# Kernel optimization log

Hardware: AMD Instinct MI355X
Metric: run time of the kernel (lower is better)

The kernel has to match this reference:

```python
import jax, jax.numpy as jnp
import numpy as np

N, E = 50000, 800000
H, C = 4, 32          # heads, channels -> concat dim 128
ED = 8                # edge_dim
NREL = 16             # n_relations
LAYERS = 3
MLP_HID = 100
NEG_SLOPE = 0.2


def setup_inputs():
    key = jax.random.key(0)
    ks = jax.random.split(key, 16)
    s = 0.1
    return {
        "x": jax.random.normal(ks[0], (N, 1), jnp.float32),
        "edge_index": jax.random.randint(ks[1], (2, E), 0, N),
        "edge_type": jax.random.randint(ks[2], (E,), 0, NREL),
        "edge_emb": jax.random.normal(ks[3], (NREL, ED), jnp.float32) * s,
        "W_l0": jax.random.normal(ks[4], (C, H * C), jnp.float32) * s,
        "W_l1": jax.random.normal(ks[5], (H * C, H * C), jnp.float32) * s,
        "W_l2": jax.random.normal(ks[6], (H * C, H * C), jnp.float32) * s,
        "att_src": jax.random.normal(ks[7], (LAYERS, H, C), jnp.float32) * s,
        "att_dst": jax.random.normal(ks[8], (LAYERS, H, C), jnp.float32) * s,
        "att_edge": jax.random.normal(ks[9], (LAYERS, H, C), jnp.float32) * s,
        "W_edge": jax.random.normal(ks[10], (LAYERS, ED, H * C), jnp.float32) * s,
        "bias": jax.random.normal(ks[11], (LAYERS, H * C), jnp.float32) * s,
        "mlp_W1": jax.random.normal(ks[12], (H * C, MLP_HID), jnp.float32) * s,
        "mlp_b1": jnp.zeros((MLP_HID,), jnp.float32),
        "mlp_W2": jax.random.normal(ks[13], (MLP_HID, 1), jnp.float32) * s,
        "mlp_b2": jnp.zeros((1,), jnp.float32),
    }


def _gat_layer(x, src, dst, edge_attr, W, a_src, a_dst, a_edge, We, b):
    # PyG GATConv: shared lin for src/dst, additive attention + edge attr term
    n = x.shape[0]
    h = (x @ W).reshape(n, H, C)                      # [N,H,C]
    e = (edge_attr @ We).reshape(-1, H, C)            # [E',H,C]
    s_src = (h * a_src).sum(-1)                       # [N,H]
    s_dst = (h * a_dst).sum(-1)                       # [N,H]
    s_edge = (e * a_edge).sum(-1)                     # [E',H]
    alpha = jax.nn.leaky_relu(s_src[src] + s_dst[dst] + s_edge, NEG_SLOPE)
    # softmax over incoming edges of each destination node
    amax = jax.ops.segment_max(alpha, dst, num_segments=n)
    ealpha = jnp.exp(alpha - amax[dst])
    denom = jax.ops.segment_sum(ealpha, dst, num_segments=n)
    alpha = ealpha / (denom[dst] + 1e-16)             # [E',H]
    msg = h[src] * alpha[:, :, None]                  # [E',H,C]
    out = jax.ops.segment_sum(msg, dst, num_segments=n)
    return out.reshape(n, H * C) + b


def _forward(x, edge_index, edge_type, edge_emb, W_l0, W_l1, W_l2,
             att_src, att_dst, att_edge, W_edge, bias,
             mlp_W1, mlp_b1, mlp_W2, mlp_b2):
    n = x.shape[0]
    x = jnp.broadcast_to(x, (n, C))                   # x.expand(-1, channels)
    src, dst = edge_index[0], edge_index[1]
    loop = jnp.arange(n)
    src_f = jnp.concatenate([src, loop])              # add_self_loops
    dst_f = jnp.concatenate([dst, loop])
    Ws = [W_l0, W_l1, W_l2]
    for i in range(LAYERS):
        edge_attr = edge_emb[edge_type]               # [E,ED]
        fill = jnp.broadcast_to(edge_attr.mean(0), (n, ED))  # fill_value='mean'
        edge_attr_f = jnp.concatenate([edge_attr, fill], axis=0)
        xl = x
        x = _gat_layer(x, src_f, dst_f, edge_attr_f, Ws[i],
                       att_src[i], att_dst[i], att_edge[i], W_edge[i], bias[i])
        if i > 0:
            x = x + xl                                # residual (i>0 only)
        x = jax.nn.relu(x)                            # nonlin; norm='none'
    h = jax.nn.relu(x @ mlp_W1 + mlp_b1)
    return jax.nn.sigmoid(h @ mlp_W2 + mlp_b2)        # [N,1]


def reference(x, edge_index, edge_type, edge_emb, W_l0, W_l1, W_l2,
              att_src, att_dst, att_edge, W_edge, bias,
              mlp_W1, mlp_b1, mlp_W2, mlp_b2):
    return _forward(x, edge_index, edge_type, edge_emb, W_l0, W_l1, W_l2,
                    att_src, att_dst, att_edge, W_edge, bias,
                    mlp_W1, mlp_b1, mlp_W2, mlp_b2)
```

## Files before the change

kernel.cpp:

```cpp
#include <hip/hip_runtime.h>
#include <hip/hip_bf16.h>
#include <hip/hip_fp16.h>

#define HCONC 128
#define NHEAD 4
#define CCH   32
#define EDIM  8
#define NREL  16
#define BCAP  5120
#define TILE  2048

typedef float floatx2 __attribute__((ext_vector_type(2)));
typedef short bf16x8 __attribute__((ext_vector_type(8)));
typedef float f32x4 __attribute__((ext_vector_type(4)));

__device__ inline unsigned short pack_fp8x2(float a, float b) {
    return (unsigned short)(__builtin_amdgcn_cvt_pk_fp8_f32(a, b, 0, false) & 0xFFFF);
}
__device__ inline unsigned pack_bf2(float lo, float hi) {
    __hip_bfloat162 v;
    v.x = __float2bfloat16(lo);
    v.y = __float2bfloat16(hi);
    return *(unsigned*)&v;
}

__global__ __launch_bounds__(256) void binA_kernel(
    const int* __restrict__ ei, const int* __restrict__ etype, int E, int nbuk, int nA,
    int* __restrict__ gcursor, int* __restrict__ cnt, unsigned* __restrict__ ebuf,
    const float* __restrict__ W_l1, const float* __restrict__ W_l2,
    const float* __restrict__ mW1,
    unsigned* __restrict__ Wl1q, unsigned* __restrict__ Wl2q, unsigned* __restrict__ W1q,
    const float* __restrict__ W_l0, const float* __restrict__ emb,
    const float* __restrict__ att_src, const float* __restrict__ att_dst,
    const float* __restrict__ att_edge, const float* __restrict__ W_edge,
    float* __restrict__ W0s, float* __restrict__ SA0, float* __restrict__ SD0,
    float* __restrict__ stab) {
    __shared__ int hist[256], lbase[256], gbase[256], tmp[256];
    __shared__ int lcnt16[NREL];
    __shared__ unsigned srt[TILE];
    __shared__ unsigned char sbuk[TILE];
    __shared__ float W0s_s[HCONC];
    int t = threadIdx.x;

    if ((int)blockIdx.x >= nA) {
        int pb = (int)blockIdx.x - nA;
        if (pb == 92) {
            if (t < HCONC) {
                float s = 0.f;
                for (int k = 0; k < CCH; k++) s += W_l0[k * HCONC + t];
                W0s[t] = s; W0s_s[t] = s;
            }
            __syncthreads();
            if (t < NHEAD) {
                float sa = 0.f, sd = 0.f;
                for (int c = 0; c < CCH; c++) {
                    sa += W0s_s[t * CCH + c] * att_src[t * CCH + c];
                    sd += W0s_s[t * CCH + c] * att_dst[t * CCH + c];
                }
                SA0[t] = sa; SD0[t] = sd;
            }
            if (t < 192) {
                int l = t >> 6, rem = t & 63, typ = rem >> 2, hh = rem & 3;
                const float* attr = emb + typ * EDIM;
                const float* We = W_edge + l * EDIM * HCONC;
                const float* ae = att_edge + l * HCONC + hh * CCH;
                float s = 0.f;
                for (int c = 0; c < CCH; c++) {
                    float ev = 0.f;
                    for (int dd = 0; dd < EDIM; dd++)
                        ev += attr[dd] * We[dd * HCONC + hh * CCH + c];
                    s += ev * ae[c];
                }
                stab[l * 68 + typ * 4 + hh] = s;
            }
            return;
        }
        int i = pb * 256 + t;
        if (i < 16384) {
            const float* W = (i < 8192) ? W_l1 : W_l2;
            unsigned* dst = (i < 8192) ? Wl1q : Wl2q;
            int r = i & 8191;
            int j2 = r & 3, lane = (r >> 2) & 63, kb = (r >> 8) & 3, tt = r >> 10;
            int k0 = kb * 32 + ((lane >> 4) & 3) * 8 + 2 * j2;
            int c = 16 * tt + (lane & 15);
            dst[r] = pack_bf2(W[k0 * 128 + c], W[(k0 + 1) * 128 + c]);
        } else if (i < 16384 + 7168) {
            int r = i - 16384;
            int j2 = r & 3, lane = (r >> 2) & 63, kb = (r >> 8) & 3, tt = r >> 10;
            int k0 = kb * 32 + ((lane >> 4) & 3) * 8 + 2 * j2;
            int c = 16 * tt + (lane & 15);
            float lo = (c < 100) ? mW1[k0 * 100 + c] : 0.f;
            float hi = (c < 100) ? mW1[(k0 + 1) * 100 + c] : 0.f;
            W1q[r] = pack_bf2(lo, hi);
        }
        return;
    }

    hist[t] = 0;
    if (t < NREL) lcnt16[t] = 0;
    __syncthreads();

    int base = blockIdx.x * TILE;
    int count = min(TILE, E - base);

    unsigned rec[8]; int slot[8]; int buk[8];
#pragma unroll
    for (int i = 0; i < 8; i++) {
        int idx = t + i * 256;
        if (idx < count) {
            int g = base + idx;
            int s = ei[g], d = ei[E + g], ty = etype[g];
            rec[i] = (unsigned)s | ((unsigned)ty << 16) | ((unsigned)(d & 255) << 20);
            buk[i] = d >> 8;
            slot[i] = atomicAdd(&hist[buk[i]], 1);
            atomicAdd(&lcnt16[ty], 1);
        } else buk[i] = -1;
    }
    __syncthreads();

    int v = hist[t];
    tmp[t] = v; __syncthreads();
    for (int off = 1; off < 256; off <<= 1) {
        int add = (t >= off) ? tmp[t - off] : 0; __syncthreads();
        tmp[t] += add; __syncthreads();
    }
    lbase[t] = tmp[t] - v;
    if (t < nbuk && v > 0) gbase[t] = atomicAdd(&gcursor[t], v);
    __syncthreads();

#pragma unroll
    for (int i = 0; i < 8; i++)
        if (buk[i] >= 0) {
            int pos = lbase[buk[i]] + slot[i];
            srt[pos] = rec[i];
            sbuk[pos] = (unsigned char)buk[i];
        }
    if (t < NREL) atomicAdd(&cnt[t], lcnt16[t]);
    __syncthreads();

    for (int idx = t; idx < count; idx += 256) {
        unsigned r = srt[idx];
        int bk = sbuk[idx];
        int rel = gbase[bk] + idx - lbase[bk];
        if (rel < BCAP) ebuf[bk * BCAP + rel] = r;
    }
}

__global__ __launch_bounds__(256) void binB_kernel(
    const unsigned* __restrict__ ebuf, const int* __restrict__ gcursor,
    int n, int nbuk,
    int* __restrict__ row_ptr, unsigned* __restrict__ col,
    const int* __restrict__ cnt, float* __restrict__ stab, int E,
    const float* __restrict__ x,
    const float* __restrict__ SA0, const float* __restrict__ SD0,
    float* __restrict__ val0) {
    __shared__ int hist[256], lcur[256], tmp[256];
    __shared__ unsigned colsl[BCAP];
    __shared__ __align__(16) float stab0[68];
    int b = blockIdx.x, t = threadIdx.x;

    if (t < 64) stab0[t] = stab[t];
    float invE = 1.f / (float)E;
    if (t < 4) {
        float s = 0.f;
        for (int r = 0; r < NREL; r++) s += (float)cnt[r] * stab[r * 4 + t];
        stab0[64 + t] = s * invE;
    }

    int c = (t < nbuk) ? gcursor[t] : 0;
    tmp[t] = c; __syncthreads();
    for (int off = 1; off < 256; off <<= 1) {
        int add = (t >= off) ? tmp[t - off] : 0; __syncthreads();
        tmp[t] += add; __syncthreads();
    }
    int gstart = (b == 0) ? 0 : tmp[b - 1];
    if (b == 0 && t == nbuk - 1) row_ptr[n] = tmp[t];
    if (b == 0 && t < 12) {
        int l = t >> 2, hh = t & 3;
        float s = 0.f;
        for (int r = 0; r < NREL; r++) s += (float)cnt[r] * stab[l * 68 + r * 4 + hh];
        stab[l * 68 + 64 + hh] = s * invE;
    }
    __syncthreads();

    int bbase = b * BCAP;
    int cntb = min(gcursor[b], BCAP);
    hist[t] = 0;
    __syncthreads();
    for (int i = t; i < cntb; i += 256) {
        unsigned r = ebuf[bbase + i];
        atomicAdd(&hist[r >> 20], 1);
    }
    __syncthreads();
    int v = hist[t];
    tmp[t] = v; __syncthreads();
    for (int off = 1; off < 256; off <<= 1) {
        int add = (t >= off) ? tmp[t - off] : 0; __syncthreads();
        tmp[t] += add; __syncthreads();
    }
    lcur[t] = tmp[t] - v;
    int gdst = (b << 8) + t;
    if (gdst < n) row_ptr[gdst] = gstart + tmp[t] - v;
    __syncthreads();
    for (int i = t; i < cntb; i += 256) {
        unsigned r = ebuf[bbase + i];
        int pos = atomicAdd(&lcur[r >> 20], 1);
        colsl[pos] = r & 0xFFFFFu;
    }
    __syncthreads();
    for (int i = t; i < cntb; i += 256)
        col[gstart + i] = colsl[i];

    int lo = tmp[t] - v, hi = tmp[t];
    if (gdst < n) {
        float xd = x[gdst];
        float4 sa4 = *(const float4*)SA0;
        float4 sdc = *(const float4*)SD0;
        float sd0 = xd * sdc.x, sd1 = xd * sdc.y, sd2 = xd * sdc.z, sd3 = xd * sdc.w;
        float s0 = fmaf(xd, sa4.x, sd0) + stab0[64];
        float s1 = fmaf(xd, sa4.y, sd1) + stab0[65];
        float s2 = fmaf(xd, sa4.z, sd2) + stab0[66];
        float s3 = fmaf(xd, sa4.w, sd3) + stab0[67];
        s0 = s0 > 0.f ? s0 : 0.2f * s0;
        s1 = s1 > 0.f ? s1 : 0.2f * s1;
        s2 = s2 > 0.f ? s2 : 0.2f * s2;
        s3 = s3 > 0.f ? s3 : 0.2f * s3;
        float w0 = __expf(s0), w1 = __expf(s1), w2 = __expf(s2), w3 = __expf(s3);
        float den0 = w0, den1 = w1, den2 = w2, den3 = w3;
        float sx0 = w0 * xd, sx1 = w1 * xd, sx2 = w2 * xd, sx3 = w3 * xd;
        for (int j = lo; j < hi; j++) {
            unsigned p = colsl[j];
            float xv = x[p & 0xFFFFu];
            int typ = (int)(p >> 16);
            float4 st = *(const float4*)&stab0[typ * 4];
            float e0 = fmaf(xv, sa4.x, sd0) + st.x;
            float e1 = fmaf(xv, sa4.y, sd1) + st.y;
            float e2 = fmaf(xv, sa4.z, sd2) + st.z;
            float e3 = fmaf(xv, sa4.w, sd3) + st.w;
            e0 = e0 > 0.f ? e0 : 0.2f * e0;
            e1 = e1 > 0.f ? e1 : 0.2f * e1;
            e2 = e2 > 0.f ? e2 : 0.2f * e2;
            e3 = e3 > 0.f ? e3 : 0.2f * e3;
            float g0 = __expf(e0), g1 = __expf(e1), g2 = __expf(e2), g3 = __expf(e3);
            den0 += g0; den1 += g1; den2 += g2; den3 += g3;
            sx0 = fmaf(g0, xv, sx0); sx1 = fmaf(g1, xv, sx1);
            sx2 = fmaf(g2, xv, sx2); sx3 = fmaf(g3, xv, sx3);
        }
        float4 vo;
        vo.x = sx0 / (den0 + 1e-16f);
        vo.y = sx1 / (den1 + 1e-16f);
        vo.z = sx2 / (den2 + 1e-16f);
        vo.w = sx3 / (den3 + 1e-16f);
        ((float4*)val0)[gdst] = vo;
    }
}

__global__ __launch_bounds__(256, 2) void transform0_kernel(
    const float* __restrict__ val0, const float* __restrict__ W0s,
    const float* __restrict__ bias0, const unsigned* __restrict__ Wq,
    const float* __restrict__ a_src, const float* __restrict__ a_dst,
    unsigned short* __restrict__ h8, float* __restrict__ s_src,
    float* __restrict__ s_dst, int n) {
    __shared__ unsigned short hs[64 * 128];
    int tid = threadIdx.x;
    int lane = tid & 63;
    int wv = tid >> 6;
    int q = lane >> 4, nl = lane & 15;
    int row_blk = blockIdx.x * 64;
    int wrow = wv * 16;

    int arow = row_blk + wrow + nl;
    if (arow >= n) arow = n - 1;
    float4 v4 = ((const float4*)val0)[arow];

    f32x4 acc[8];
#pragma unroll
    for (int t = 0; t < 8; t++) acc[t] = (f32x4){0.f, 0.f, 0.f, 0.f};

    const uint4* Wp4 = (const uint4*)Wq;
#pragma unroll
    for (int kb = 0; kb < 4; kb++) {
        int c4 = 8 * kb + 2 * q;
        float4 wa = ((const float4*)W0s)[c4];
        float4 wb = ((const float4*)W0s)[c4 + 1];
        float4 ba = ((const float4*)bias0)[c4];
        float4 bb = ((const float4*)bias0)[c4 + 1];
        float vr = kb == 0 ? v4.x : kb == 1 ? v4.y : kb == 2 ? v4.z : v4.w;
        float x0 = fmaxf(fmaf(vr, wa.x, ba.x), 0.f);
        float x1 = fmaxf(fmaf(vr, wa.y, ba.y), 0.f);
        float x2 = fmaxf(fmaf(vr, wa.z, ba.z), 0.f);
        float x3 = fmaxf(fmaf(vr, wa.w, ba.w), 0.f);
        float x4 = fmaxf(fmaf(vr, wb.x, bb.x), 0.f);
        float x5 = fmaxf(fmaf(vr, wb.y, bb.y), 0.f);
        float x6 = fmaxf(fmaf(vr, wb.z, bb.z), 0.f);
        float x7 = fmaxf(fmaf(vr, wb.w, bb.w), 0.f);
        uint4 ua;
        ua.x = pack_bf2(x0, x1);
        ua.y = pack_bf2(x2, x3);
        ua.z = pack_bf2(x4, x5);
        ua.w = pack_bf2(x6, x7);
        bf16x8 af = __builtin_bit_cast(bf16x8, ua);
#pragma unroll
        for (int t = 0; t < 8; t++) {
            uint4 ub = Wp4[(t * 4 + kb) * 64 + lane];
            bf16x8 bf = __builtin_bit_cast(bf16x8, ub);
            acc[t] = __builtin_amdgcn_mfma_f32_16x16x32_bf16(af, bf, acc[t], 0, 0, 0);
        }
    }

    float av[8], dv[8];
#pragma unroll
    for (int t = 0; t < 8; t++) {
        av[t] = a_src[16 * t + nl];
        dv[t] = a_dst[16 * t + nl];
    }
#pragma unroll
    for (int reg = 0; reg < 4; reg++) {
        float t0 = acc[0][reg] * av[0] + acc[1][reg] * av[1];
        float t1 = acc[2][reg] * av[2] + acc[3][reg] * av[3];
        float t2 = acc[4][reg] * av[4] + acc[5][reg] * av[5];
        float t3 = acc[6][reg] * av[6] + acc[7][reg] * av[7];
        float d0 = acc[0][reg] * dv[0] + acc[1][reg] * dv[1];
        float d1 = acc[2][reg] * dv[2] + acc[3][reg] * dv[3];
        float d2 = acc[4][reg] * dv[4] + acc[5][reg] * dv[5];
        float d3 = acc[6][reg] * dv[6] + acc[7][reg] * dv[7];
#pragma unroll
        for (int off = 1; off <= 8; off <<= 1) {
            t0 += __shfl_xor(t0, off); t1 += __shfl_xor(t1, off);
            t2 += __shfl_xor(t2, off); t3 += __shfl_xor(t3, off);
            d0 += __shfl_xor(d0, off); d1 += __shfl_xor(d1, off);
            d2 += __shfl_xor(d2, off); d3 += __shfl_xor(d3, off);
        }
        int row = row_blk + wrow + q * 4 + reg;
        if (row < n && nl < 4) {
            float ts = nl == 0 ? t0 : nl == 1 ? t1 : nl == 2 ? t2 : t3;
            float td = nl == 0 ? d0 : nl == 1 ? d1 : nl == 2 ? d2 : d3;
            s_src[row * 4 + nl] = ts;
            s_dst[row * 4 + nl] = td;
        }
    }

#pragma unroll
    for (int t = 0; t < 8; t++) {
#pragma unroll
        for (int reg = 0; reg < 4; reg++) {
            __hip_bfloat16 b = __float2bfloat16(acc[t][reg]);
            hs[(wrow + q * 4 + reg) * 128 + 16 * t + nl] = *(unsigned short*)&b;
        }
    }
    __syncthreads();
    const unsigned* hsu = (const unsigned*)hs;
#pragma unroll
    for (int i = 0; i < 16; i++) {
        int pidx = tid + i * 256;
        int rl = pidx >> 6, cp = pidx & 63;
        int row = row_blk + rl;
        if (row < n) {
            unsigned u = hsu[rl * 64 + cp];
            float f0 = __uint_as_float(u << 16);
            float f1 = __uint_as_float(u & 0xFFFF0000u);
            h8[(size_t)row * 64 + cp] = pack_fp8x2(f0, f1);
        }
    }
}

__global__ __launch_bounds__(256, 2) void transform_kernel(
    const unsigned short* __restrict__ Xbf, const unsigned* __restrict__ Wq,
    const float* __restrict__ a_src, const float* __restrict__ a_dst,
    unsigned short* __restrict__ h8, float* __restrict__ s_src,
    float* __restrict__ s_dst, int n) {
    __shared__ unsigned short hs[64 * 128];
    int tid = threadIdx.x;
    int lane = tid & 63;
    int wv = tid >> 6;
    int q = lane >> 4, nl = lane & 15;
    int row_blk = blockIdx.x * 64;
    int wrow = wv * 16;

    int arow = row_blk + wrow + nl;
    if (arow >= n) arow = n - 1;
    const uint4* Xr = (const uint4*)(Xbf + (size_t)arow * HCONC);

    f32x4 acc[8];
#pragma unroll
    for (int t = 0; t < 8; t++) acc[t] = (f32x4){0.f, 0.f, 0.f, 0.f};

    const uint4* Wp4 = (const uint4*)Wq;
#pragma unroll
    for (int kb = 0; kb < 4; kb++) {
        uint4 ua = Xr[kb * 4 + q];
        bf16x8 af = __builtin_bit_cast(bf16x8, ua);
#pragma unroll
        for (int t = 0; t < 8; t++) {
            uint4 ub = Wp4[(t * 4 + kb) * 64 + lane];
            bf16x8 bf = __builtin_bit_cast(bf16x8, ub);
            acc[t] = __builtin_amdgcn_mfma_f32_16x16x32_bf16(af, bf, acc[t], 0, 0, 0);
        }
    }

    float av[8], dv[8];
#pragma unroll
    for (int t = 0; t < 8; t++) {
        av[t] = a_src[16 * t + nl];
        dv[t] = a_dst[16 * t + nl];
    }
#pragma unroll
    for (int reg = 0; reg < 4; reg++) {
        float t0 = acc[0][reg] * av[0] + acc[1][reg] * av[1];
        float t1 = acc[2][reg] * av[2] + acc[3][reg] * av[3];
        float t2 = acc[4][reg] * av[4] + acc[5][reg] * av[5];
        float t3 = acc[6][reg] * av[6] + acc[7][reg] * av[7];
        float d0 = acc[0][reg] * dv[0] + acc[1][reg] * dv[1];
        float d1 = acc[2][reg] * dv[2] + acc[3][reg] * dv[3];
        float d2 = acc[4][reg] * dv[4] + acc[5][reg] * dv[5];
        float d3 = acc[6][reg] * dv[6] + acc[7][reg] * dv[7];
#pragma unroll
        for (int off = 1; off <= 8; off <<= 1) {
            t0 += __shfl_xor(t0, off); t1 += __shfl_xor(t1, off);
            t2 += __shfl_xor(t2, off); t3 += __shfl_xor(t3, off);
            d0 += __shfl_xor(d0, off); d1 += __shfl_xor(d1, off);
            d2 += __shfl_xor(d2, off); d3 += __shfl_xor(d3, off);
        }
        int row = row_blk + wrow + q * 4 + reg;
        if (row < n && nl < 4) {
            float ts = nl == 0 ? t0 : nl == 1 ? t1 : nl == 2 ? t2 : t3;
            float td = nl == 0 ? d0 : nl == 1 ? d1 : nl == 2 ? d2 : d3;
            s_src[row * 4 + nl] = ts;
            s_dst[row * 4 + nl] = td;
        }
    }

#pragma unroll
    for (int t = 0; t < 8; t++) {
#pragma unroll
        for (int reg = 0; reg < 4; reg++) {
            __hip_bfloat16 b = __float2bfloat16(acc[t][reg]);
            hs[(wrow + q * 4 + reg) * 128 + 16 * t + nl] = *(unsigned short*)&b;
        }
    }
    __syncthreads();
    const unsigned* hsu = (const unsigned*)hs;
#pragma unroll
    for (int i = 0; i < 16; i++) {
        int pidx = tid + i * 256;
        int rl = pidx >> 6, cp = pidx & 63;
        int row = row_blk + rl;
        if (row < n) {
            unsigned u = hsu[rl * 64 + cp];
            float f0 = __uint_as_float(u << 16);
            float f1 = __uint_as_float(u & 0xFFFF0000u);
            h8[(size_t)row * 64 + cp] = pack_fp8x2(f0, f1);
        }
    }
}

template <bool VAL_RES, bool OUT_BF16, bool RES_BF16>
__global__ __launch_bounds__(256) void agg_kernel(
    const unsigned char* __restrict__ h8,
    const float* __restrict__ s_src, const float* __restrict__ s_dst,
    const int* __restrict__ row_ptr, const unsigned* __restrict__ col,
    const float* __restrict__ tab, const float* __restrict__ bias,
    const void* __restrict__ x_prev,
    const float* __restrict__ val0, const float* __restrict__ W0s,
    const float* __restrict__ bias0,
    void* __restrict__ x_out, int n) {
    __shared__ __align__(16) float stab_s[68];
    if (threadIdx.x < 68) stab_s[threadIdx.x] = tab[threadIdx.x];
    __syncthreads();

    int tid = threadIdx.x;
    int lane = tid & 63;
    int grp = lane >> 4;
    int l16 = lane & 15;
    int head = l16 >> 2;
    int d = blockIdx.x * 16 + (tid >> 6) * 4 + grp;
    if (d >= n) return;

    int start = row_ptr[d], end = row_ptr[d + 1];
    float sdh = s_dst[d * 4 + head];

    float s = s_src[d * 4 + head] + sdh + stab_s[64 + head];
    s = s > 0.f ? s : 0.2f * s;
    float w = __expf(s);
    uint2 u = ((const uint2*)(h8 + (size_t)d * 128))[l16];
    floatx2 f01 = __builtin_amdgcn_cvt_pk_f32_fp8((int)u.x, false);
    floatx2 f23 = __builtin_amdgcn_cvt_pk_f32_fp8((int)u.x, true);
    floatx2 f45 = __builtin_amdgcn_cvt_pk_f32_fp8((int)u.y, false);
    floatx2 f67 = __builtin_amdgcn_cvt_pk_f32_fp8((int)u.y, true);
    float den = w;
    float a0 = w * f01.x, a1 = w * f01.y;
    float a2 = w * f23.x, a3 = w * f23.y;
    float a4 = w * f45.x, a5 = w * f45.y;
    float a6 = w * f67.x, a7 = w * f67.y;

#pragma unroll 4
    for (int e = start; e < end; e++) {
        unsigned pp = col[e];
        int esrc = (int)(pp & 0xFFFFu);
        int typ = (int)(pp >> 16);
        float ss = s_src[esrc * 4 + head];
        float sc = ss + sdh + stab_s[typ * 4 + head];
        sc = sc > 0.f ? sc : 0.2f * sc;
        float we = __expf(sc);
        uint2 ue = ((const uint2*)(h8 + (size_t)esrc * 128))[l16];
        floatx2 g01 = __builtin_amdgcn_cvt_pk_f32_fp8((int)ue.x, false);
        floatx2 g23 = __builtin_amdgcn_cvt_pk_f32_fp8((int)ue.x, true);
        floatx2 g45 = __builtin_amdgcn_cvt_pk_f32_fp8((int)ue.y, false);
        floatx2 g67 = __builtin_amdgcn_cvt_pk_f32_fp8((int)ue.y, true);
        den += we;
        a0 = fmaf(we, g01.x, a0);  a1 = fmaf(we, g01.y, a1);
        a2 = fmaf(we, g23.x, a2);  a3 = fmaf(we, g23.y, a3);
        a4 = fmaf(we, g45.x, a4);  a5 = fmaf(we, g45.y, a5);
        a6 = fmaf(we, g67.x, a6);  a7 = fmaf(we, g67.y, a7);
    }

    float inv = 1.f / (den + 1e-16f);
    float4 b0 = ((const float4*)bias)[2 * l16];
    float4 b1v = ((const float4*)bias)[2 * l16 + 1];
    float4 o0v, o1v;
    o0v.x = a0 * inv + b0.x;  o0v.y = a1 * inv + b0.y;
    o0v.z = a2 * inv + b0.z;  o0v.w = a3 * inv + b0.w;
    o1v.x = a4 * inv + b1v.x; o1v.y = a5 * inv + b1v.y;
    o1v.z = a6 * inv + b1v.z; o1v.w = a7 * inv + b1v.w;
    if (VAL_RES) {
        float vv = val0[d * 4 + head];
        float4 wa = ((const float4*)W0s)[2 * l16];
        float4 wb = ((const float4*)W0s)[2 * l16 + 1];
        float4 ba = ((const float4*)bias0)[2 * l16];
        float4 bb = ((const float4*)bias0)[2 * l16 + 1];
        o0v.x += fmaxf(fmaf(vv, wa.x, ba.x), 0.f);
        o0v.y += fmaxf(fmaf(vv, wa.y, ba.y), 0.f);
        o0v.z += fmaxf(fmaf(vv, wa.z, ba.z), 0.f);
        o0v.w += fmaxf(fmaf(vv, wa.w, ba.w), 0.f);
        o1v.x += fmaxf(fmaf(vv, wb.x, bb.x), 0.f);
        o1v.y += fmaxf(fmaf(vv, wb.y, bb.y), 0.f);
        o1v.z += fmaxf(fmaf(vv, wb.z, bb.z), 0.f);
        o1v.w += fmaxf(fmaf(vv, wb.w, bb.w), 0.f);
    } else if (RES_BF16) {
        uint4 pk = ((const uint4*)x_prev)[(size_t)d * 16 + l16];
        o0v.x += __uint_as_float(pk.x << 16);
        o0v.y += __uint_as_float(pk.x & 0xFFFF0000u);
        o0v.z += __uint_as_float(pk.y << 16);
        o0v.w += __uint_as_float(pk.y & 0xFFFF0000u);
        o1v.x += __uint_as_float(pk.z << 16);
        o1v.y += __uint_as_float(pk.z & 0xFFFF0000u);
        o1v.z += __uint_as_float(pk.w << 16);
        o1v.w += __uint_as_float(pk.w & 0xFFFF0000u);
    }
    o0v.x = fmaxf(o0v.x, 0.f); o0v.y = fmaxf(o0v.y, 0.f);
    o0v.z = fmaxf(o0v.z, 0.f); o0v.w = fmaxf(o0v.w, 0.f);
    o1v.x = fmaxf(o1v.x, 0.f); o1v.y = fmaxf(o1v.y, 0.f);
    o1v.z = fmaxf(o1v.z, 0.f); o1v.w = fmaxf(o1v.w, 0.f);
    if (OUT_BF16) {
        uint4 pk;
        pk.x = pack_bf2(o0v.x, o0v.y);
        pk.y = pack_bf2(o0v.z, o0v.w);
        pk.z = pack_bf2(o1v.x, o1v.y);
        pk.w = pack_bf2(o1v.z, o1v.w);
        ((uint4*)x_out)[(size_t)d * 16 + l16] = pk;
    } else {
        ((float4*)x_out)[(size_t)d * 32 + 2 * l16]     = o0v;
        ((float4*)x_out)[(size_t)d * 32 + 2 * l16 + 1] = o1v;
    }
}

__global__ __launch_bounds__(256, 2) void mlp_kernel(
    const unsigned short* __restrict__ Xbf, const unsigned* __restrict__ W1q,
    const float* __restrict__ b1, const float* __restrict__ W2,
    const float* __restrict__ b2, float* __restrict__ out, int n) {
    int tid = threadIdx.x;
    int lane = tid & 63;
    int wv = tid >> 6;
    int q = lane >> 4, nl = lane & 15;
    int row_blk = blockIdx.x * 64;
    int wrow = wv * 16;

    int arow = row_blk + wrow + nl;
    if (arow >= n) arow = n - 1;
    const uint4* Xr = (const uint4*)(Xbf + (size_t)arow * HCONC);

    f32x4 acc[7];
#pragma unroll
    for (int t = 0; t < 7; t++) acc[t] = (f32x4){0.f, 0.f, 0.f, 0.f};

    const uint4* Wp4 = (const uint4*)W1q;
#pragma unroll
    for (int kb = 0; kb < 4; kb++) {
        uint4 ua = Xr[kb * 4 + q];
        bf16x8 af = __builtin_bit_cast(bf16x8, ua);
#pragma unroll
        for (int t = 0; t < 7; t++) {
            uint4 ub = Wp4[(t * 4 + kb) * 64 + lane];
            bf16x8 bf = __builtin_bit_cast(bf16x8, ub);
            acc[t] = __builtin_amdgcn_mfma_f32_16x16x32_bf16(af, bf, acc[t], 0, 0, 0);
        }
    }

    float b1c[7], w2c[7];
#pragma unroll
    for (int t = 0; t < 7; t++) {
        int c = 16 * t + nl;
        bool vld = c < 100;
        b1c[t] = vld ? b1[c] : 0.f;
        w2c[t] = vld ? W2[c] : 0.f;
    }
    float b2v = b2[0];

#pragma unroll
    for (int reg = 0; reg < 4; reg++) {
        float sum = 0.f;
#pragma unroll
        for (int t = 0; t < 7; t++) {
            float hv = fmaxf(acc[t][reg] + b1c[t], 0.f);
            sum = fmaf(hv, w2c[t], sum);
        }
#pragma unroll
        for (int off = 1; off <= 8; off <<= 1)
            sum += __shfl_xor(sum, off);
        int row = row_blk + wrow + q * 4 + reg;
        if (nl == 0 && row < n)
            out[row] = 1.f / (1.f + __expf(-(sum + b2v)));
    }
}

extern "C" void kernel_launch(void* const* d_in, const int* in_sizes, int n_in,
                              void* d_out, int out_size, void* d_ws, size_t ws_size,
                              hipStream_t stream) {
    const float* x       = (const float*)d_in[0];
    const int*   ei      = (const int*)d_in[1];
    const int*   etype   = (const int*)d_in[2];
    const float* emb     = (const float*)d_in[3];
    const float* W_l0    = (const float*)d_in[4];
    const float* W_l1    = (const float*)d_in[5];
    const float* W_l2    = (const float*)d_in[6];
    const float* att_src = (const float*)d_in[7];
    const float* att_dst = (const float*)d_in[8];
    const float* att_edge= (const float*)d_in[9];
    const float* W_edge  = (const float*)d_in[10];
    const float* bias    = (const float*)d_in[11];
    const float* mW1     = (const float*)d_in[12];
    const float* mb1     = (const float*)d_in[13];
    const float* mW2     = (const float*)d_in[14];
    const float* mb2     = (const float*)d_in[15];

    int n = in_sizes[0];
    int E = in_sizes[2];
    int nbuk = (n + 255) >> 8;
    int nA = (E + TILE - 1) / TILE;

    float* p   = (float*)d_ws;
    float* xa  = p; p += (size_t)n * HCONC;
    float* xb  = p; p += (size_t)n * HCONC;
    float* ssrc = p; p += (size_t)n * NHEAD;
    float* sdst = p; p += (size_t)n * NHEAD;
    float* val0 = p; p += (size_t)n * NHEAD;
    float* hbf  = p; p += (size_t)n * 32;
    unsigned* Wl1q = (unsigned*)p; p += 8192;
    unsigned* Wl2q = (unsigned*)p; p += 8192;
    unsigned* W1q  = (unsigned*)p; p += 7168;
    int* row_ptr     = (int*)p;
    int* gcursor     = row_ptr + n + 1;
    int* cnt         = gcursor + 256;
    float* W0s    = (float*)(cnt + 16);
    float* SA0    = W0s + HCONC;
    float* SD0    = SA0 + NHEAD;
    float* meanat = SD0 + NHEAD;
    float* stab   = meanat + EDIM;
    char* raw = (char*)(stab + 256);
    unsigned* ebuf = (unsigned*)(((uintptr_t)raw + 15) & ~(uintptr_t)15);
    unsigned* col = ebuf + (size_t)nbuk * BCAP;

    hipMemsetAsync(gcursor, 0, (256 + 16) * sizeof(int), stream);
    binA_kernel<<<nA + 93, 256, 0, stream>>>(ei, etype, E, nbuk, nA, gcursor, cnt,
                                             ebuf, W_l1, W_l2, mW1, Wl1q, Wl2q, W1q,
                                             W_l0, emb, att_src, att_dst, att_edge,
                                             W_edge, W0s, SA0, SD0, stab);
    binB_kernel<<<nbuk, 256, 0, stream>>>(ebuf, gcursor, n, nbuk, row_ptr, col,
                                          cnt, stab, E, x, SA0, SD0, val0);

    transform0_kernel<<<(n + 63) / 64, 256, 0, stream>>>(val0, W0s, bias + 0, Wl1q,
                                                         att_src + 128, att_dst + 128,
                                                         (unsigned short*)hbf, ssrc, sdst, n);
    agg_kernel<true, true, false><<<(n + 15) / 16, 256, 0, stream>>>(
        (const unsigned char*)hbf, ssrc, sdst, row_ptr, col,
        stab + 68, bias + 128, nullptr, val0, W0s, bias + 0, xb, n);
    transform_kernel<<<(n + 63) / 64, 256, 0, stream>>>((const unsigned short*)xb, Wl2q,
                                                        att_src + 256, att_dst + 256,
                                                        (unsigned short*)hbf, ssrc, sdst, n);
    agg_kernel<false, true, true><<<(n + 15) / 16, 256, 0, stream>>>(
        (const unsigned char*)hbf, ssrc, sdst, row_ptr, col,
        stab + 136, bias + 256, xb, nullptr, nullptr, nullptr, xa, n);
    mlp_kernel<<<(n + 63) / 64, 256, 0, stream>>>((const unsigned short*)xa, W1q,
                                                  mb1, mW2, mb2, (float*)d_out, n);
}
```

Before: 220.4 us.

## Fuse layer-2 transform into agg epilogue and MLP into final aggregation

The layer-1 aggregation kernel now stages its 16 output rows in shared memory and immediately runs the layer-2 MFMA transform, attention-score reduction and fp8 packing. This removes the separate transform kernel and its re-read of the bf16 activations. The final aggregation likewise computes the MLP head and sigmoid in-block, dropping the xa buffer and the mlp kernel. Separate double buffers for h8 and the scores avoid read/write hazards between blocks. The trade-offs are extra syncthreads and more shared memory per block in the latency-bound gather kernels, plus 16-row MFMA tiles that reload weights more often.

```diff
diff --git a/kernel.cpp b/kernel.cpp
--- a/kernel.cpp
+++ b/kernel.cpp
@@ -364,125 +364,42 @@
     }
 }
 
-__global__ __launch_bounds__(256, 2) void transform_kernel(
-    const unsigned short* __restrict__ Xbf, const unsigned* __restrict__ Wq,
-    const float* __restrict__ a_src, const float* __restrict__ a_dst,
-    unsigned short* __restrict__ h8, float* __restrict__ s_src,
-    float* __restrict__ s_dst, int n) {
-    __shared__ unsigned short hs[64 * 128];
+__global__ __launch_bounds__(256) void agg_t_kernel(
+    const unsigned char* __restrict__ h8, const float* __restrict__ s_src,
+    const float* __restrict__ s_dst, const int* __restrict__ row_ptr,
+    const unsigned* __restrict__ col, const float* __restrict__ tab,
+    const float* __restrict__ bias, const float* __restrict__ val0,
+    const float* __restrict__ W0s, const float* __restrict__ bias0,
+    unsigned short* __restrict__ xb_out,
+    const unsigned* __restrict__ Wq,
+    const float* __restrict__ a_src2, const float* __restrict__ a_dst2,
+    unsigned short* __restrict__ h8o, float* __restrict__ s_srco,
+    float* __restrict__ s_dsto, int n) {
+    __shared__ __align__(16) float stab_s[68];
+    __shared__ __align__(16) unsigned short xrow[16 * 144];
+    __shared__ __align__(4) unsigned short hs[16 * 130];
+    if (threadIdx.x < 68) stab_s[threadIdx.x] = tab[threadIdx.x];
+    __syncthreads();
+
     int tid = threadIdx.x;
     int lane = tid & 63;
     int wv = tid >> 6;
-    int q = lane >> 4, nl = lane & 15;
-    int row_blk = blockIdx.x * 64;
-    int wrow = wv * 16;
-
-    int arow = row_blk + wrow + nl;
-    if (arow >= n) arow = n - 1;
-    const uint4* Xr = (const uint4*)(Xbf + (size_t)arow * HCONC);
-
-    f32x4 acc[8];
-#pragma unroll
-    for (int t = 0; t < 8; t++) acc[t] = (f32x4){0.f, 0.f, 0.f, 0.f};
-
-    const uint4* Wp4 = (const uint4*)Wq;
-#pragma unroll
-    for (int kb = 0; kb < 4; kb++) {
-        uint4 ua = Xr[kb * 4 + q];
-        bf16x8 af = __builtin_bit_cast(bf16x8, ua);
-#pragma unroll
-        for (int t = 0; t < 8; t++) {
-            uint4 ub = Wp4[(t * 4 + kb) * 64 + lane];
-            bf16x8 bf = __builtin_bit_cast(bf16x8, ub);
-            acc[t] = __builtin_amdgcn_mfma_f32_16x16x32_bf16(af, bf, acc[t], 0, 0, 0);
-        }
-    }
-
-    float av[8], dv[8];
-#pragma unroll
-    for (int t = 0; t < 8; t++) {
-        av[t] = a_src[16 * t + nl];
-        dv[t] = a_dst[16 * t + nl];
-    }
-#pragma unroll
-    for (int reg = 0; reg < 4; reg++) {
-        float t0 = acc[0][reg] * av[0] + acc[1][reg] * av[1];
-        float t1 = acc[2][reg] * av[2] + acc[3][reg] * av[3];
-        float t2 = acc[4][reg] * av[4] + acc[5][reg] * av[5];
-        float t3 = acc[6][reg] * av[6] + acc[7][reg] * av[7];
-        float d0 = acc[0][reg] * dv[0] + acc[1][reg] * dv[1];
-        float d1 = acc[2][reg] * dv[2] + acc[3][reg] * dv[3];
-        float d2 = acc[4][reg] * dv[4] + acc[5][reg] * dv[5];
-        float d3 = acc[6][reg] * dv[6] + acc[7][reg] * dv[7];
-#pragma unroll
-        for (int off = 1; off <= 8; off <<= 1) {
-            t0 += __shfl_xor(t0, off); t1 += __shfl_xor(t1, off);
-            t2 += __shfl_xor(t2, off); t3 += __shfl_xor(t3, off);
-            d0 += __shfl_xor(d0, off); d1 += __shfl_xor(d1, off);
-            d2 += __shfl_xor(d2, off); d3 += __shfl_xor(d3, off);
-        }
-        int row = row_blk + wrow + q * 4 + reg;
-        if (row < n && nl < 4) {
-            float ts = nl == 0 ? t0 : nl == 1 ? t1 : nl == 2 ? t2 : t3;
-            float td = nl == 0 ? d0 : nl == 1 ? d1 : nl == 2 ? d2 : d3;
-            s_src[row * 4 + nl] = ts;
-            s_dst[row * 4 + nl] = td;
-        }
-    }
-
-#pragma unroll
-    for (int t = 0; t < 8; t++) {
-#pragma unroll
-        for (int reg = 0; reg < 4; reg++) {
-            __hip_bfloat16 b = __float2bfloat16(acc[t][reg]);
-            hs[(wrow + q * 4 + reg) * 128 + 16 * t + nl] = *(unsigned short*)&b;
-        }
-    }
-    __syncthreads();
-    const unsigned* hsu = (const unsigned*)hs;
-#pragma unroll
-    for (int i = 0; i < 16; i++) {
-        int pidx = tid + i * 256;
-        int rl = pidx >> 6, cp = pidx & 63;
-        int row = row_blk + rl;
-        if (row < n) {
-            unsigned u = hsu[rl * 64 + cp];
-            float f0 = __uint_as_float(u << 16);
-            float f1 = __uint_as_float(u & 0xFFFF0000u);
-            h8[(size_t)row * 64 + cp] = pack_fp8x2(f0, f1);
-        }
-    }
-}
-
-template <bool VAL_RES, bool OUT_BF16, bool RES_BF16>
-__global__ __launch_bounds__(256) void agg_kernel(
-    const unsigned char* __restrict__ h8,
-    const float* __restrict__ s_src, const float* __restrict__ s_dst,
-    const int* __restrict__ row_ptr, const unsigned* __restrict__ col,
-    const float* __restrict__ tab, const float* __restrict__ bias,
-    const void* __restrict__ x_prev,
-    const float* __restrict__ val0, const float* __restrict__ W0s,
-    const float* __restrict__ bias0,
-    void* __restrict__ x_out, int n) {
-    __shared__ __align__(16) float stab_s[68];
-    if (threadIdx.x < 68) stab_s[threadIdx.x] = tab[threadIdx.x];
-    __syncthreads();
-
-    int tid = threadIdx.x;
-    int lane = tid & 63;
     int grp = lane >> 4;
     int l16 = lane & 15;
     int head = l16 >> 2;
-    int d = blockIdx.x * 16 + (tid >> 6) * 4 + grp;
-    if (d >= n) return;
-
-    int start = row_ptr[d], end = row_ptr[d + 1];
-    float sdh = s_dst[d * 4 + head];
-
-    float s = s_src[d * 4 + head] + sdh + stab_s[64 + head];
+    int dl = wv * 4 + grp;
+    int d = blockIdx.x * 16 + dl;
+    bool alive = d < n;
+    int dc = alive ? d : n - 1;
+
+    int start = row_ptr[dc];
+    int end = alive ? row_ptr[dc + 1] : start;
+    float sdh = s_dst[dc * 4 + head];
+
+    float s = s_src[dc * 4 + head] + sdh + stab_s[64 + head];
     s = s > 0.f ? s : 0.2f * s;
     float w = __expf(s);
-    uint2 u = ((const uint2*)(h8 + (size_t)d * 128))[l16];
+    uint2 u = ((const uint2*)(h8 + (size_t)dc * 128))[l16];
     floatx2 f01 = __builtin_amdgcn_cvt_pk_f32_fp8((int)u.x, false);
     floatx2 f23 = __builtin_amdgcn_cvt_pk_f32_fp8((int)u.x, true);
     floatx2 f45 = __builtin_amdgcn_cvt_pk_f32_fp8((int)u.y, false);
@@ -492,14 +409,12 @@
     float a2 = w * f23.x, a3 = w * f23.y;
     float a4 = w * f45.x, a5 = w * f45.y;
     float a6 = w * f67.x, a7 = w * f67.y;
-
 #pragma unroll 4
     for (int e = start; e < end; e++) {
         unsigned pp = col[e];
         int esrc = (int)(pp & 0xFFFFu);
         int typ = (int)(pp >> 16);
-        float ss = s_src[esrc * 4 + head];
-        float sc = ss + sdh + stab_s[typ * 4 + head];
+        float sc = s_src[esrc * 4 + head] + sdh + stab_s[typ * 4 + head];
         sc = sc > 0.f ? sc : 0.2f * sc;
         float we = __expf(sc);
         uint2 ue = ((const uint2*)(h8 + (size_t)esrc * 128))[l16];
@@ -522,8 +437,8 @@
     o0v.z = a2 * inv + b0.z;  o0v.w = a3 * inv + b0.w;
     o1v.x = a4 * inv + b1v.x; o1v.y = a5 * inv + b1v.y;
     o1v.z = a6 * inv + b1v.z; o1v.w = a7 * inv + b1v.w;
-    if (VAL_RES) {
-        float vv = val0[d * 4 + head];
+    {
+        float vv = val0[dc * 4 + head];
         float4 wa = ((const float4*)W0s)[2 * l16];
         float4 wb = ((const float4*)W0s)[2 * l16 + 1];
         float4 ba = ((const float4*)bias0)[2 * l16];
@@ -536,90 +451,204 @@
         o1v.y += fmaxf(fmaf(vv, wb.y, bb.y), 0.f);
         o1v.z += fmaxf(fmaf(vv, wb.z, bb.z), 0.f);
         o1v.w += fmaxf(fmaf(vv, wb.w, bb.w), 0.f);
-    } else if (RES_BF16) {
-        uint4 pk = ((const uint4*)x_prev)[(size_t)d * 16 + l16];
-        o0v.x += __uint_as_float(pk.x << 16);
-        o0v.y += __uint_as_float(pk.x & 0xFFFF0000u);
-        o0v.z += __uint_as_float(pk.y << 16);
-        o0v.w += __uint_as_float(pk.y & 0xFFFF0000u);
-        o1v.x += __uint_as_float(pk.z << 16);
-        o1v.y += __uint_as_float(pk.z & 0xFFFF0000u);
-        o1v.z += __uint_as_float(pk.w << 16);
-        o1v.w += __uint_as_float(pk.w & 0xFFFF0000u);
     }
     o0v.x = fmaxf(o0v.x, 0.f); o0v.y = fmaxf(o0v.y, 0.f);
     o0v.z = fmaxf(o0v.z, 0.f); o0v.w = fmaxf(o0v.w, 0.f);
     o1v.x = fmaxf(o1v.x, 0.f); o1v.y = fmaxf(o1v.y, 0.f);
     o1v.z = fmaxf(o1v.z, 0.f); o1v.w = fmaxf(o1v.w, 0.f);
-    if (OUT_BF16) {
-        uint4 pk;
-        pk.x = pack_bf2(o0v.x, o0v.y);
-        pk.y = pack_bf2(o0v.z, o0v.w);
-        pk.z = pack_bf2(o1v.x, o1v.y);
-        pk.w = pack_bf2(o1v.z, o1v.w);
-        ((uint4*)x_out)[(size_t)d * 16 + l16] = pk;
-    } else {
-        ((float4*)x_out)[(size_t)d * 32 + 2 * l16]     = o0v;
-        ((float4*)x_out)[(size_t)d * 32 + 2 * l16 + 1] = o1v;
+    uint4 pk;
+    pk.x = pack_bf2(o0v.x, o0v.y);
+    pk.y = pack_bf2(o0v.z, o0v.w);
+    pk.z = pack_bf2(o1v.x, o1v.y);
+    pk.w = pack_bf2(o1v.z, o1v.w);
+    if (alive) ((uint4*)xb_out)[(size_t)d * 16 + l16] = pk;
+    *(uint4*)&xrow[dl * 144 + l16 * 8] = pk;
+    __syncthreads();
+
+    int lo = 2 * wv, hi = lo + 1;
+    f32x4 aL = (f32x4){0.f, 0.f, 0.f, 0.f};
+    f32x4 aH = (f32x4){0.f, 0.f, 0.f, 0.f};
+    const uint4* Wp4 = (const uint4*)Wq;
+#pragma unroll
+    for (int kb = 0; kb < 4; kb++) {
+        bf16x8 af = __builtin_bit_cast(bf16x8,
+            *(const uint4*)&xrow[l16 * 144 + kb * 32 + grp * 8]);
+        bf16x8 bL = __builtin_bit_cast(bf16x8, Wp4[(lo * 4 + kb) * 64 + lane]);
+        bf16x8 bH = __builtin_bit_cast(bf16x8, Wp4[(hi * 4 + kb) * 64 + lane]);
+        aL = __builtin_amdgcn_mfma_f32_16x16x32_bf16(af, bL, aL, 0, 0, 0);
+        aH = __builtin_amdgcn_mfma_f32_16x16x32_bf16(af, bH, aH, 0, 0, 0);
+    }
+    float avl = a_src2[32 * wv + l16], avh = a_src2[32 * wv + 16 + l16];
+    float dvl = a_dst2[32 * wv + l16], dvh = a_dst2[32 * wv + 16 + l16];
+#pragma unroll
+    for (int reg = 0; reg < 4; reg++) {
+        float ps = aL[reg] * avl + aH[reg] * avh;
+        float pd = aL[reg] * dvl + aH[reg] * dvh;
+#pragma unroll
+        for (int off = 1; off <= 8; off <<= 1) {
+            ps += __shfl_xor(ps, off);
+            pd += __shfl_xor(pd, off);
+        }
+        int rg = blockIdx.x * 16 + grp * 4 + reg;
+        if (l16 == 0 && rg < n) {
+            s_srco[rg * 4 + wv] = ps;
+            s_dsto[rg * 4 + wv] = pd;
+        }
+        __hip_bfloat16 bLh = __float2bfloat16(aL[reg]);
+        __hip_bfloat16 bHh = __float2bfloat16(aH[reg]);
+        hs[(grp * 4 + reg) * 130 + 16 * lo + l16] = *(unsigned short*)&bLh;
+        hs[(grp * 4 + reg) * 130 + 16 * hi + l16] = *(unsigned short*)&bHh;
+    }
+    __syncthreads();
+#pragma unroll
+    for (int i = 0; i < 4; i++) {
+        int pidx = tid + i * 256;
+        int rl = pidx >> 6, cp = pidx & 63;
+        int rg = blockIdx.x * 16 + rl;
+        if (rg < n) {
+            unsigned uu = *(const unsigned*)&hs[rl * 130 + cp * 2];
+            float f0 = __uint_as_float(uu << 16);
+            float f1 = __uint_as_float(uu & 0xFFFF0000u);
+            h8o[(size_t)rg * 64 + cp] = pack_fp8x2(f0, f1);
+        }
     }
 }
 
-__global__ __launch_bounds__(256, 2) void mlp_kernel(
-    const unsigned short* __restrict__ Xbf, const unsigned* __restrict__ W1q,
-    const float* __restrict__ b1, const float* __restrict__ W2,
-    const float* __restrict__ b2, float* __restrict__ out, int n) {
+__global__ __launch_bounds__(256) void agg_m_kernel(
+    const unsigned char* __restrict__ h8, const float* __restrict__ s_src,
+    const float* __restrict__ s_dst, const int* __restrict__ row_ptr,
+    const unsigned* __restrict__ col, const float* __restrict__ tab,
+    const float* __restrict__ bias, const unsigned short* __restrict__ x_prev,
+    const unsigned* __restrict__ W1q, const float* __restrict__ b1,
+    const float* __restrict__ W2, const float* __restrict__ b2,
+    float* __restrict__ out, int n) {
+    __shared__ __align__(16) float stab_s[68];
+    __shared__ __align__(16) unsigned short xrow[16 * 144];
+    __shared__ float partial[16][4];
+    if (threadIdx.x < 68) stab_s[threadIdx.x] = tab[threadIdx.x];
+    __syncthreads();
+
     int tid = threadIdx.x;
     int lane = tid & 63;
     int wv = tid >> 6;
-    int q = lane >> 4, nl = lane & 15;
-    int row_blk = blockIdx.x * 64;
-    int wrow = wv * 16;
-
-    int arow = row_blk + wrow + nl;
-    if (arow >= n) arow = n - 1;
-    const uint4* Xr = (const uint4*)(Xbf + (size_t)arow * HCONC);
-
-    f32x4 acc[7];
-#pragma unroll
-    for (int t = 0; t < 7; t++) acc[t] = (f32x4){0.f, 0.f, 0.f, 0.f};
-
+    int grp = lane >> 4;
+    int l16 = lane & 15;
+    int head = l16 >> 2;
+    int dl = wv * 4 + grp;
+    int d = blockIdx.x * 16 + dl;
+    bool alive = d < n;
+    int dc = alive ? d : n - 1;
+
+    int start = row_ptr[dc];
+    int end = alive ? row_ptr[dc + 1] : start;
+    float sdh = s_dst[dc * 4 + head];
+
+    float s = s_src[dc * 4 + head] + sdh + stab_s[64 + head];
+    s = s > 0.f ? s : 0.2f * s;
+    float w = __expf(s);
+    uint2 u = ((const uint2*)(h8 + (size_t)dc * 128))[l16];
+    floatx2 f01 = __builtin_amdgcn_cvt_pk_f32_fp8((int)u.x, false);
+    floatx2 f23 = __builtin_amdgcn_cvt_pk_f32_fp8((int)u.x, true);
+    floatx2 f45 = __builtin_amdgcn_cvt_pk_f32_fp8((int)u.y, false);
+    floatx2 f67 = __builtin_amdgcn_cvt_pk_f32_fp8((int)u.y, true);
+    float den = w;
+    float a0 = w * f01.x, a1 = w * f01.y;
+    float a2 = w * f23.x, a3 = w * f23.y;
+    float a4 = w * f45.x, a5 = w * f45.y;
+    float a6 = w * f67.x, a7 = w * f67.y;
+#pragma unroll 4
+    for (int e = start; e < end; e++) {
+        unsigned pp = col[e];
+        int esrc = (int)(pp & 0xFFFFu);
+        int typ = (int)(pp >> 16);
+        float sc = s_src[esrc * 4 + head] + sdh + stab_s[typ * 4 + head];
+        sc = sc > 0.f ? sc : 0.2f * sc;
+        float we = __expf(sc);
+        uint2 ue = ((const uint2*)(h8 + (size_t)esrc * 128))[l16];
+        floatx2 g01 = __builtin_amdgcn_cvt_pk_f32_fp8((int)ue.x, false);
+        floatx2 g23 = __builtin_amdgcn_cvt_pk_f32_fp8((int)ue.x, true);
+        floatx2 g45 = __builtin_amdgcn_cvt_pk_f32_fp8((int)ue.y, false);
+        floatx2 g67 = __builtin_amdgcn_cvt_pk_f32_fp8((int)ue.y, true);
+        den += we;
+        a0 = fmaf(we, g01.x, a0);  a1 = fmaf(we, g01.y, a1);
+        a2 = fmaf(we, g23.x, a2);  a3 = fmaf(we, g23.y, a3);
+        a4 = fmaf(we, g45.x, a4);  a5 = fmaf(we, g45.y, a5);
+        a6 = fmaf(we, g67.x, a6);  a7 = fmaf(we, g67.y, a7);
+    }
+
+    float inv = 1.f / (den + 1e-16f);
+    float4 b0 = ((const float4*)bias)[2 * l16];
+    float4 b1v = ((const float4*)bias)[2 * l16 + 1];
+    float4 o0v, o1v;
+    o0v.x = a0 * inv + b0.x;  o0v.y = a1 * inv + b0.y;
+    o0v.z = a2 * inv + b0.z;  o0v.w = a3 * inv + b0.w;
+    o1v.x = a4 * inv + b1v.x; o1v.y = a5 * inv + b1v.y;
+    o1v.z = a6 * inv + b1v.z; o1v.w = a7 * inv + b1v.w;
+    {
+        uint4 pr = ((const uint4*)x_prev)[(size_t)dc * 16 + l16];
+        o0v.x += __uint_as_float(pr.x << 16);
+        o0v.y += __uint_as_float(pr.x & 0xFFFF0000u);
+        o0v.z += __uint_as_float(pr.y << 16);
+        o0v.w += __uint_as_float(pr.y & 0xFFFF0000u);
+        o1v.x += __uint_as_float(pr.z << 16);
+        o1v.y += __uint_as_float(pr.z & 0xFFFF0000u);
+        o1v.z += __uint_as_float(pr.w << 16);
+        o1v.w += __uint_as_float(pr.w & 0xFFFF0000u);
+    }
+    o0v.x = fmaxf(o0v.x, 0.f); o0v.y = fmaxf(o0v.y, 0.f);
+    o0v.z = fmaxf(o0v.z, 0.f); o0v.w = fmaxf(o0v.w, 0.f);
+    o1v.x = fmaxf(o1v.x, 0.f); o1v.y = fmaxf(o1v.y, 0.f);
+    o1v.z = fmaxf(o1v.z, 0.f); o1v.w = fmaxf(o1v.w, 0.f);
+    uint4 pk;
+    pk.x = pack_bf2(o0v.x, o0v.y);
+    pk.y = pack_bf2(o0v.z, o0v.w);
+    pk.z = pack_bf2(o1v.x, o1v.y);
+    pk.w = pack_bf2(o1v.z, o1v.w);
+    *(uint4*)&xrow[dl * 144 + l16 * 8] = pk;
+    __syncthreads();
+
+    int lo = 2 * wv;
+    bool two = wv < 3;
+    f32x4 aL = (f32x4){0.f, 0.f, 0.f, 0.f};
+    f32x4 aH = (f32x4){0.f, 0.f, 0.f, 0.f};
     const uint4* Wp4 = (const uint4*)W1q;
 #pragma unroll
     for (int kb = 0; kb < 4; kb++) {
-        uint4 ua = Xr[kb * 4 + q];
-        bf16x8 af = __builtin_bit_cast(bf16x8, ua);
-#pragma unroll
-        for (int t = 0; t < 7; t++) {
-            uint4 ub = Wp4[(t * 4 + kb) * 64 + lane];
-            bf16x8 bf = __builtin_bit_cast(bf16x8, ub);
-            acc[t] = __builtin_amdgcn_mfma_f32_16x16x32_bf16(af, bf, acc[t], 0, 0, 0);
-        }
-    }
-
-    float b1c[7], w2c[7];
-#pragma unroll
-    for (int t = 0; t < 7; t++) {
-        int c = 16 * t + nl;
-        bool vld = c < 100;
-        b1c[t] = vld ? b1[c] : 0.f;
-        w2c[t] = vld ? W2[c] : 0.f;
-    }
-    float b2v = b2[0];
-
+        bf16x8 af = __builtin_bit_cast(bf16x8,
+            *(const uint4*)&xrow[l16 * 144 + kb * 32 + grp * 8]);
+        bf16x8 bL = __builtin_bit_cast(bf16x8, Wp4[(lo * 4 + kb) * 64 + lane]);
+        aL = __builtin_amdgcn_mfma_f32_16x16x32_bf16(af, bL, aL, 0, 0, 0);
+        if (two) {
+            bf16x8 bH = __builtin_bit_cast(bf16x8, Wp4[((lo + 1) * 4 + kb) * 64 + lane]);
+            aH = __builtin_amdgcn_mfma_f32_16x16x32_bf16(af, bH, aH, 0, 0, 0);
+        }
+    }
+    int cL = 16 * lo + l16;
+    float b1L = (cL < 100) ? b1[cL] : 0.f;
+    float w2L = (cL < 100) ? W2[cL] : 0.f;
+    float b1H = 0.f, w2H = 0.f;
+    if (two) {
+        int cH = cL + 16;
+        b1H = (cH < 100) ? b1[cH] : 0.f;
+        w2H = (cH < 100) ? W2[cH] : 0.f;
+    }
 #pragma unroll
     for (int reg = 0; reg < 4; reg++) {
-        float sum = 0.f;
-#pragma unroll
-        for (int t = 0; t < 7; t++) {
-            float hv = fmaxf(acc[t][reg] + b1c[t], 0.f);
-            sum = fmaf(hv, w2c[t], sum);
-        }
+        float psum = fmaxf(aL[reg] + b1L, 0.f) * w2L;
+        if (two) psum = fmaf(fmaxf(aH[reg] + b1H, 0.f), w2H, psum);
 #pragma unroll
         for (int off = 1; off <= 8; off <<= 1)
-            sum += __shfl_xor(sum, off);
-        int row = row_blk + wrow + q * 4 + reg;
-        if (nl == 0 && row < n)
-            out[row] = 1.f / (1.f + __expf(-(sum + b2v)));
+            psum += __shfl_xor(psum, off);
+        if (l16 == 0) partial[grp * 4 + reg][wv] = psum;
+    }
+    __syncthreads();
+    if (tid < 16) {
+        int rg = blockIdx.x * 16 + tid;
+        if (rg < n) {
+            float sum = partial[tid][0] + partial[tid][1] +
+                        partial[tid][2] + partial[tid][3] + b2[0];
+            out[rg] = 1.f / (1.f + __expf(-sum));
+        }
     }
 }
 
@@ -649,12 +678,14 @@
     int nA = (E + TILE - 1) / TILE;
 
     float* p   = (float*)d_ws;
-    float* xa  = p; p += (size_t)n * HCONC;
-    float* xb  = p; p += (size_t)n * HCONC;
+    float* xb  = p; p += (size_t)n * 64;
     float* ssrc = p; p += (size_t)n * NHEAD;
     float* sdst = p; p += (size_t)n * NHEAD;
+    float* ssrc2 = p; p += (size_t)n * NHEAD;
+    float* sdst2 = p; p += (size_t)n * NHEAD;
     float* val0 = p; p += (size_t)n * NHEAD;
     float* hbf  = p; p += (size_t)n * 32;
+    float* hbf2 = p; p += (size_t)n * 32;
     unsigned* Wl1q = (unsigned*)p; p += 8192;
     unsigned* Wl2q = (unsigned*)p; p += 8192;
     unsigned* W1q  = (unsigned*)p; p += 7168;
@@ -670,7 +701,7 @@
     unsigned* ebuf = (unsigned*)(((uintptr_t)raw + 15) & ~(uintptr_t)15);
     unsigned* col = ebuf + (size_t)nbuk * BCAP;
 
-    hipMemsetAsync(gcursor, 0, (256 + 16) * sizeof(int), stream);
+    (void)hipMemsetAsync(gcursor, 0, (256 + 16) * sizeof(int), stream);
     binA_kernel<<<nA + 93, 256, 0, stream>>>(ei, etype, E, nbuk, nA, gcursor, cnt,
                                              ebuf, W_l1, W_l2, mW1, Wl1q, Wl2q, W1q,
                                              W_l0, emb, att_src, att_dst, att_edge,
@@ -681,15 +712,13 @@
     transform0_kernel<<<(n + 63) / 64, 256, 0, stream>>>(val0, W0s, bias + 0, Wl1q,
                                                          att_src + 128, att_dst + 128,
                                                          (unsigned short*)hbf, ssrc, sdst, n);
-    agg_kernel<true, true, false><<<(n + 15) / 16, 256, 0, stream>>>(
+    agg_t_kernel<<<(n + 15) / 16, 256, 0, stream>>>(
         (const unsigned char*)hbf, ssrc, sdst, row_ptr, col,
-        stab + 68, bias + 128, nullptr, val0, W0s, bias + 0, xb, n);
-    transform_kernel<<<(n + 63) / 64, 256, 0, stream>>>((const unsigned short*)xb, Wl2q,
-                                                        att_src + 256, att_dst + 256,
-                                                        (unsigned short*)hbf, ssrc, sdst, n);
-    agg_kernel<false, true, true><<<(n + 15) / 16, 256, 0, stream>>>(
-        (const unsigned char*)hbf, ssrc, sdst, row_ptr, col,
-        stab + 136, bias + 256, xb, nullptr, nullptr, nullptr, xa, n);
-    mlp_kernel<<<(n + 63) / 64, 256, 0, stream>>>((const unsigned short*)xa, W1q,
-                                                  mb1, mW2, mb2, (float*)d_out, n);
+        stab + 68, bias + 128, val0, W0s, bias + 0,
+        (unsigned short*)xb, Wl2q, att_src + 256, att_dst + 256,
+        (unsigned short*)hbf2, ssrc2, sdst2, n);
+    agg_m_kernel<<<(n + 15) / 16, 256, 0, stream>>>(
+        (const unsigned char*)hbf2, ssrc2, sdst2, row_ptr, col,
+        stab + 136, bias + 256, (const unsigned short*)xb,
+        W1q, mb1, mW2, mb2, (float*)d_out, n);
 }
```

New measurement: 202.7 us. -8.0%, faster.
